# Kernel optimization log

Measured on AMD Instinct MI355X. Metric: run time of the kernel, lower is better.

Reference implementation:

```python
import jax, jax.numpy as jnp
import numpy as np

EMBED = 1024
HEADS = 16
HEAD_DIM = EMBED // HEADS
SCALE = HEAD_DIM ** (-0.5)
LN_EPS = 1e-5


def setup_inputs() -> dict:
    key = jax.random.key(0)
    ks = jax.random.split(key, 8)
    B, N = 2, 2048
    s = EMBED ** -0.5
    return {
        "x": jax.random.normal(ks[0], (B, N, EMBED), dtype=jnp.float32),
        "ln_w": jnp.ones((EMBED,), jnp.float32),
        "ln_b": jnp.zeros((EMBED,), jnp.float32),
        "Wq": jax.random.normal(ks[1], (EMBED, EMBED), jnp.float32) * s,
        "Wk": jax.random.normal(ks[2], (EMBED, EMBED), jnp.float32) * s,
        "Wv": jax.random.normal(ks[3], (EMBED, EMBED), jnp.float32) * s,
        "Wo": jax.random.normal(ks[4], (EMBED, EMBED), jnp.float32) * s,
        "bo": jnp.zeros((EMBED,), jnp.float32),
    }


def reference(x, ln_w, ln_b, Wq, Wk, Wv, Wo, bo):
    residual = x
    # LayerNorm (pre-norm)
    mu = jnp.mean(x, axis=-1, keepdims=True)
    var = jnp.mean(jnp.square(x - mu), axis=-1, keepdims=True)
    xn = (x - mu) * jax.lax.rsqrt(var + LN_EPS) * ln_w + ln_b

    B, N, _ = xn.shape
    q = (xn @ Wq.T).reshape(B, N, HEADS, HEAD_DIM).transpose(0, 2, 1, 3)  # b h n d
    k = (xn @ Wk.T).reshape(B, N, HEADS, HEAD_DIM).transpose(0, 2, 1, 3)
    v = (xn @ Wv.T).reshape(B, N, HEADS, HEAD_DIM).transpose(0, 2, 1, 3)

    dots = jnp.einsum('bhqd,bhkd->bhqk', q, k) * SCALE
    causal = jnp.tril(jnp.ones((N, N), dtype=bool))
    dots = jnp.where(causal, dots, -jnp.inf)
    attn = jax.nn.softmax(dots, axis=-1)
    out = jnp.einsum('bhqk,bhkd->bhqd', attn, v)
    out = out.transpose(0, 2, 1, 3).reshape(B, N, EMBED)
    # dropout is identity in eval mode
    return residual + out @ Wo.T + bo
```

## Files before the change

kernel.cpp:

```cpp
#include <hip/hip_runtime.h>

#define E 1024
#define NSEQ 2048
#define HEADS 16
#define HD 64

typedef unsigned short u16;
typedef short short8 __attribute__((ext_vector_type(8)));
typedef float f32x4 __attribute__((ext_vector_type(4)));

template<bool B> struct BC { static constexpr bool v = B; };

#define GLOAD_LDS16(gp, lp)                                        \
    __builtin_amdgcn_global_load_lds(                              \
        (const __attribute__((address_space(1))) void*)(gp),       \
        (__attribute__((address_space(3))) void*)(lp), 16, 0, 0)

__device__ __forceinline__ u16 f2bf(float f) {
    union { float f; unsigned u; } v; v.f = f;
    unsigned r = v.u + 0x7fffu + ((v.u >> 16) & 1u);
    return (u16)(r >> 16);
}

__device__ __forceinline__ unsigned cvt_pk_bf16(float lo, float hi) {
    unsigned r;
    asm("v_cvt_pk_bf16_f32 %0, %1, %2" : "=v"(r) : "v"(lo), "v"(hi));
    return r;
}

__device__ __forceinline__ f32x4 mfma16(short8 a, short8 b, f32x4 c) {
    return __builtin_amdgcn_mfma_f32_16x16x32_bf16(a, b, c, 0, 0, 0);
}

__global__ __launch_bounds__(256) void convw_k(
    const float* __restrict__ Wq, const float* __restrict__ Wk,
    const float* __restrict__ Wv, const float* __restrict__ Wo,
    u16* __restrict__ out)
{
    const unsigned i = (blockIdx.x * 256u + threadIdx.x) * 4u;
    const unsigned m = i >> 20;
    const float* src = (m == 0) ? Wq : (m == 1) ? Wk : (m == 2) ? Wv : Wo;
    const float4 v = *(const float4*)(src + (i & 0xFFFFFu));
    *(uint2*)(out + i) = make_uint2(
        ((unsigned)f2bf(v.x)) | (((unsigned)f2bf(v.y)) << 16),
        ((unsigned)f2bf(v.z)) | (((unsigned)f2bf(v.w)) << 16));
}

__global__ __launch_bounds__(256) void ln_fwd(
    const float* __restrict__ X, const float* __restrict__ w,
    const float* __restrict__ bb, u16* __restrict__ xn)
{
    const int row = blockIdx.x, tid = threadIdx.x;
    const int lane = tid & 63, wave = tid >> 6;
    const float4 v = ((const float4*)(X + (size_t)row * E))[tid];
    float s = v.x + v.y + v.z + v.w;
    float s2 = v.x * v.x + v.y * v.y + v.z * v.z + v.w * v.w;
#pragma unroll
    for (int off = 1; off < 64; off <<= 1) {
        s += __shfl_xor(s, off);
        s2 += __shfl_xor(s2, off);
    }
    __shared__ float red[8];
    if (lane == 0) { red[wave] = s; red[4 + wave] = s2; }
    __syncthreads();
    s = red[0] + red[1] + red[2] + red[3];
    s2 = red[4] + red[5] + red[6] + red[7];
    const float mu = s * (1.f / 1024.f);
    float var = s2 * (1.f / 1024.f) - mu * mu;
    var = fmaxf(var, 0.f);
    const float rs = rsqrtf(var + 1e-5f);
    const float4 wv = ((const float4*)w)[tid];
    const float4 bv = ((const float4*)bb)[tid];
    u16 o0 = f2bf((v.x - mu) * rs * wv.x + bv.x);
    u16 o1 = f2bf((v.y - mu) * rs * wv.y + bv.y);
    u16 o2 = f2bf((v.z - mu) * rs * wv.z + bv.z);
    u16 o3 = f2bf((v.w - mu) * rs * wv.w + bv.w);
    *(uint2*)(xn + (size_t)row * E + tid * 4) =
        make_uint2(((unsigned)o0) | (((unsigned)o1) << 16),
                   ((unsigned)o2) | (((unsigned)o3) << 16));
}

__global__ __launch_bounds__(256) void vtrans(
    const u16* __restrict__ Vb, u16* __restrict__ VT)
{
    __shared__ u16 tl[64][65];
    const int t = threadIdx.x;
    const int ntile = blockIdx.x, bh = blockIdx.y;
    const int b = bh >> 4, h = bh & 15;
    const int n0 = ntile * 64;
    {
        const int nl = t >> 2;
        const u16* src = Vb + ((size_t)b * NSEQ + n0 + nl) * E + h * 64;
#pragma unroll
        for (int u = 0; u < 2; ++u) {
            const int d0 = (t & 3) * 16 + u * 8;
            short8 v = *(const short8*)(src + d0);
#pragma unroll
            for (int j = 0; j < 8; ++j) tl[nl][d0 + j] = (u16)v[j];
        }
    }
    __syncthreads();
    {
        const int d = t >> 2, nc = (t & 3) * 16;
        u16* dst = VT + ((size_t)bh * 64 + d) * NSEQ + n0 + nc;
#pragma unroll
        for (int u = 0; u < 2; ++u) {
            short8 o;
#pragma unroll
            for (int j = 0; j < 8; ++j) o[j] = (short)tl[nc + u * 8 + j][d];
            *(short8*)(dst + u * 8) = o;
        }
    }
}

template<int MODE>
__global__ __launch_bounds__(256) void gemm_nt(
    const u16* __restrict__ A, const u16* __restrict__ Wbase,
    u16* __restrict__ outb, float* __restrict__ outf,
    const float* __restrict__ resid, const float* __restrict__ bias)
{
    __shared__ __align__(16) unsigned char As[128 * 128];
    __shared__ __align__(16) unsigned char Bs[128 * 128];
    const int tid = threadIdx.x;
    const int lane = tid & 63, wave = tid >> 6;
    const int l15 = lane & 15, l4 = lane >> 4;
    const int wm = wave >> 1, wn = wave & 1;
    const int nt = blockIdx.x, mt = blockIdx.y, z = blockIdx.z;
    const u16* Bw = Wbase + (size_t)z * (E * (size_t)E);

    const int lrow8 = lane >> 3;
    const int lchunk = (lane & 7) ^ lrow8;
    const u16* gA = A + (size_t)(mt * 128 + lrow8) * E + lchunk * 8;
    const u16* gB = Bw + (size_t)(nt * 128 + lrow8) * E + lchunk * 8;

    f32x4 acc[4][4] = {};

    for (int kt = 0; kt < 16; ++kt) {
#pragma unroll
        for (int i = 0; i < 4; ++i) {
            const int rb = (i * 4 + wave) * 8;
            GLOAD_LDS16(gA + (size_t)rb * E + kt * 64, As + rb * 128);
            GLOAD_LDS16(gB + (size_t)rb * E + kt * 64, Bs + rb * 128);
        }
        __syncthreads();
#pragma unroll
        for (int ks = 0; ks < 2; ++ks) {
            short8 af[4], bfr[4];
#pragma unroll
            for (int i = 0; i < 4; ++i) {
                int ra = wm * 64 + i * 16 + l15;
                af[i] = *(const short8*)(As + ra * 128 + ((ks * 64 + l4 * 16) ^ ((ra & 7) << 4)));
                int rb2 = wn * 64 + i * 16 + l15;
                bfr[i] = *(const short8*)(Bs + rb2 * 128 + ((ks * 64 + l4 * 16) ^ ((rb2 & 7) << 4)));
            }
#pragma unroll
            for (int i = 0; i < 4; ++i)
#pragma unroll
                for (int j = 0; j < 4; ++j)
                    acc[i][j] = mfma16(af[i], bfr[j], acc[i][j]);
        }
        __syncthreads();
    }

    const int orow0 = mt * 128 + wm * 64, ocol0 = nt * 128 + wn * 64;
    if (MODE == 0) {
        u16* outz = outb + (size_t)z * (4096 * (size_t)E);
        const float osc = (z == 0) ? 0.18033688f : 1.0f;
#pragma unroll
        for (int i = 0; i < 4; ++i)
#pragma unroll
            for (int j = 0; j < 4; ++j)
#pragma unroll
                for (int r = 0; r < 4; ++r) {
                    int row = orow0 + i * 16 + l4 * 4 + r;
                    int col = ocol0 + j * 16 + l15;
                    outz[(size_t)row * E + col] = f2bf(acc[i][j][r] * osc);
                }
    } else {
#pragma unroll
        for (int i = 0; i < 4; ++i)
#pragma unroll
            for (int j = 0; j < 4; ++j)
#pragma unroll
                for (int r = 0; r < 4; ++r) {
                    int row = orow0 + i * 16 + l4 * 4 + r;
                    int col = ocol0 + j * 16 + l15;
                    size_t idx = (size_t)row * E + col;
                    outf[idx] = acc[i][j][r] + resid[idx] + bias[col];
                }
    }
}

__global__ __launch_bounds__(256) void attn_fwd(
    const u16* __restrict__ Q, const u16* __restrict__ K,
    const u16* __restrict__ VT, u16* __restrict__ O)
{
    __shared__ __align__(16) unsigned char Kls[2 * 8192];
    __shared__ __align__(16) unsigned char Vls[2 * 8192];
    __shared__ __align__(16) unsigned char Ps[4 * 4096];
    const int tid = threadIdx.x, lane = tid & 63, wave = tid >> 6;
    const int l15 = lane & 15, l4 = lane >> 4;
    const int h = blockIdx.x, x = blockIdx.y, b = blockIdx.z;
    const int qe = b ? (15 - x) : x;
    const int qw0 = qe * 128 + wave * 32;
    const size_t bbase = (size_t)b * NSEQ * E + h * HD;
    const u16* vt = VT + ((size_t)(b * 16 + h) * 64) * NSEQ;
    const int ntiles = 2 * qe + 2;

    short8 aq[2][2];
#pragma unroll
    for (int qt = 0; qt < 2; ++qt)
#pragma unroll
        for (int ks = 0; ks < 2; ++ks)
            aq[qt][ks] = *(const short8*)(Q + bbase + (size_t)(qw0 + qt * 16 + l15) * E + ks * 32 + l4 * 8);

    f32x4 accO[2][4] = {};
    float mrow[2] = {-1e30f, -1e30f};
    float lrow[2] = {0.f, 0.f};

    unsigned char* Pw = Ps + wave * 4096;

    const int srow = lane >> 3;
    const int sc8 = ((lane & 7) ^ srow) * 8;
    auto stage = [&](int t, int buf) {
        const u16* Kg = K + bbase + (size_t)(t * 64) * E;
        const u16* vg = vt + t * 64;
        unsigned char* kd = Kls + buf * 8192 + wave * 1024;
        unsigned char* vd = Vls + buf * 8192 + wave * 1024;
#pragma unroll
        for (int i = 0; i < 2; ++i) {
            const int r = wave * 8 + srow + i * 32;
            GLOAD_LDS16(Kg + (size_t)r * E + sc8, kd + i * 4096);
            GLOAD_LDS16(vg + (size_t)r * NSEQ + sc8, vd + i * 4096);
        }
    };

    stage(0, 0);
    __syncthreads();

    auto step = [&](int t, auto mc) {
        constexpr bool MASK = decltype(mc)::v;
        const int buf = t & 1;
        if (t + 1 < ntiles) stage(t + 1, buf ^ 1);
        const unsigned char* Kc = Kls + buf * 8192;
        const unsigned char* Vc = Vls + buf * 8192;

        f32x4 s[2][4] = {};
#pragma unroll
        for (int kvt = 0; kvt < 4; ++kvt) {
            const int kr = kvt * 16 + l15;
#pragma unroll
            for (int ks = 0; ks < 2; ++ks) {
                short8 kfr = *(const short8*)(Kc + kr * 128 + ((ks * 64 + l4 * 16) ^ ((kr & 7) << 4)));
                s[0][kvt] = mfma16(kfr, aq[0][ks], s[0][kvt]);
                s[1][kvt] = mfma16(kfr, aq[1][ks], s[1][kvt]);
            }
        }

        if constexpr (MASK) {
#pragma unroll
            for (int qt = 0; qt < 2; ++qt) {
                const int qg = qw0 + qt * 16 + l15;
#pragma unroll
                for (int kvt = 0; kvt < 4; ++kvt)
#pragma unroll
                    for (int r = 0; r < 4; ++r) {
                        int kvg = t * 64 + kvt * 16 + l4 * 4 + r;
                        if (kvg > qg) s[qt][kvt][r] = -1e30f;
                    }
            }
        }

#pragma unroll
        for (int qt = 0; qt < 2; ++qt) {
            float m0 = fmaxf(fmaxf(s[qt][0][0], s[qt][0][1]), fmaxf(s[qt][0][2], s[qt][0][3]));
            float m1 = fmaxf(fmaxf(s[qt][1][0], s[qt][1][1]), fmaxf(s[qt][1][2], s[qt][1][3]));
            float m2 = fmaxf(fmaxf(s[qt][2][0], s[qt][2][1]), fmaxf(s[qt][2][2], s[qt][2][3]));
            float m3 = fmaxf(fmaxf(s[qt][3][0], s[qt][3][1]), fmaxf(s[qt][3][2], s[qt][3][3]));
            float pm = fmaxf(fmaxf(m0, m1), fmaxf(m2, m3));
            if (__any(pm > mrow[qt] + 8.f)) {
                pm = fmaxf(pm, __shfl_xor(pm, 16));
                pm = fmaxf(pm, __shfl_xor(pm, 32));
                const float mn = fmaxf(mrow[qt], pm);
                const float sc = exp2f(mrow[qt] - mn);
                mrow[qt] = mn;
                lrow[qt] *= sc;
#pragma unroll
                for (int r = 0; r < 4; ++r) {
                    float scv = __shfl(sc, l4 * 4 + r);
#pragma unroll
                    for (int dt = 0; dt < 4; ++dt) accO[qt][dt][r] *= scv;
                }
            }
            const int pr = qt * 16 + l15;
            const int sw = (l15 & 7) << 4;
#pragma unroll
            for (int kvt = 0; kvt < 4; ++kvt) {
                float p0 = exp2f(s[qt][kvt][0] - mrow[qt]);
                float p1 = exp2f(s[qt][kvt][1] - mrow[qt]);
                float p2 = exp2f(s[qt][kvt][2] - mrow[qt]);
                float p3 = exp2f(s[qt][kvt][3] - mrow[qt]);
                lrow[qt] += (p0 + p1) + (p2 + p3);
                uint2 pk = make_uint2(cvt_pk_bf16(p0, p1), cvt_pk_bf16(p2, p3));
                *(uint2*)(Pw + pr * 128 + ((kvt * 32 + l4 * 8) ^ sw)) = pk;
            }
        }

#pragma unroll
        for (int ks2 = 0; ks2 < 2; ++ks2) {
            const int cb = ks2 * 64 + l4 * 16;
            short8 pf0 = *(const short8*)(Pw + l15 * 128 + (cb ^ ((l15 & 7) << 4)));
            short8 pf1 = *(const short8*)(Pw + (16 + l15) * 128 + (cb ^ ((l15 & 7) << 4)));
#pragma unroll
            for (int dt = 0; dt < 4; ++dt) {
                const int vr = dt * 16 + l15;
                short8 vfr = *(const short8*)(Vc + vr * 128 + (cb ^ ((vr & 7) << 4)));
                accO[0][dt] = mfma16(pf0, vfr, accO[0][dt]);
                accO[1][dt] = mfma16(pf1, vfr, accO[1][dt]);
            }
        }
        __syncthreads();
    };

    int t = 0;
    for (; t < 2 * qe; ++t) step(t, BC<false>{});
    step(t, BC<true>{}); ++t;
    step(t, BC<true>{});

    float linv[2];
#pragma unroll
    for (int qt = 0; qt < 2; ++qt) {
        float tl2 = lrow[qt];
        tl2 += __shfl_xor(tl2, 16);
        tl2 += __shfl_xor(tl2, 32);
        linv[qt] = 1.f / tl2;
    }
#pragma unroll
    for (int rt = 0; rt < 2; ++rt)
#pragma unroll
        for (int r = 0; r < 4; ++r) {
            float lq = __shfl(linv[rt], l4 * 4 + r);
            const int qg = qw0 + rt * 16 + l4 * 4 + r;
#pragma unroll
            for (int dt = 0; dt < 4; ++dt)
                O[bbase + (size_t)qg * E + dt * 16 + l15] = f2bf(accO[rt][dt][r] * lq);
        }
}

extern "C" void kernel_launch(void* const* d_in, const int* in_sizes, int n_in,
                              void* d_out, int out_size, void* d_ws, size_t ws_size,
                              hipStream_t stream)
{
    const float* x    = (const float*)d_in[0];
    const float* ln_w = (const float*)d_in[1];
    const float* ln_b = (const float*)d_in[2];
    const float* Wq   = (const float*)d_in[3];
    const float* Wk   = (const float*)d_in[4];
    const float* Wv   = (const float*)d_in[5];
    const float* Wo   = (const float*)d_in[6];
    const float* bo   = (const float*)d_in[7];
    float* out = (float*)d_out;

    u16* ws  = (u16*)d_ws;
    u16* Wbf = ws;
    u16* xn  = Wbf + (size_t)4 * 1024 * 1024;
    u16* Qb  = xn + (size_t)4096 * 1024;
    u16* Kb  = Qb + (size_t)4096 * 1024;
    u16* Vb  = Kb + (size_t)4096 * 1024;
    u16* Ob  = Vb + (size_t)4096 * 1024;
    u16* VT  = xn;

    convw_k<<<dim3(4096), dim3(256), 0, stream>>>(Wq, Wk, Wv, Wo, Wbf);
    ln_fwd<<<dim3(4096), dim3(256), 0, stream>>>(x, ln_w, ln_b, xn);
    gemm_nt<0><<<dim3(8, 32, 3), dim3(256), 0, stream>>>(
        xn, Wbf, Qb, nullptr, nullptr, nullptr);
    vtrans<<<dim3(32, 32), dim3(256), 0, stream>>>(Vb, VT);
    attn_fwd<<<dim3(16, 16, 2), dim3(256), 0, stream>>>(Qb, Kb, VT, Ob);
    gemm_nt<1><<<dim3(8, 32, 1), dim3(256), 0, stream>>>(
        Ob, Wbf + (size_t)3 * 1024 * 1024, nullptr, out, x, bo);
}
```

Measured before the change: 132.6 us.

## Split KV range across wave pairs and pair causal strips per block

```diff
diff --git a/kernel.cpp b/kernel.cpp
--- a/kernel.cpp
+++ b/kernel.cpp
@@ -195,156 +195,197 @@
     const u16* __restrict__ Q, const u16* __restrict__ K,
     const u16* __restrict__ VT, u16* __restrict__ O)
 {
-    __shared__ __align__(16) unsigned char Kls[2 * 8192];
-    __shared__ __align__(16) unsigned char Vls[2 * 8192];
+    __shared__ __align__(16) unsigned char Kls[2 * 16384];
+    __shared__ __align__(16) unsigned char Vls[2 * 16384];
     __shared__ __align__(16) unsigned char Ps[4 * 4096];
     const int tid = threadIdx.x, lane = tid & 63, wave = tid >> 6;
+    const int sub = wave >> 1, par = wave & 1;
     const int l15 = lane & 15, l4 = lane >> 4;
-    const int h = blockIdx.x, x = blockIdx.y, b = blockIdx.z;
-    const int qe = b ? (15 - x) : x;
-    const int qw0 = qe * 128 + wave * 32;
+    const int h = blockIdx.x, j = blockIdx.y, b = blockIdx.z;
     const size_t bbase = (size_t)b * NSEQ * E + h * HD;
     const u16* vt = VT + ((size_t)(b * 16 + h) * 64) * NSEQ;
-    const int ntiles = 2 * qe + 2;
-
-    short8 aq[2][2];
-#pragma unroll
-    for (int qt = 0; qt < 2; ++qt)
-#pragma unroll
-        for (int ks = 0; ks < 2; ++ks)
-            aq[qt][ks] = *(const short8*)(Q + bbase + (size_t)(qw0 + qt * 16 + l15) * E + ks * 32 + l4 * 8);
-
-    f32x4 accO[2][4] = {};
-    float mrow[2] = {-1e30f, -1e30f};
-    float lrow[2] = {0.f, 0.f};
 
     unsigned char* Pw = Ps + wave * 4096;
-
-    const int srow = lane >> 3;
-    const int sc8 = ((lane & 7) ^ srow) * 8;
+    const int srowK = lane >> 3, kchunk = (lane & 7) ^ srowK;
+    const int srowV = lane >> 4, vchunk = (lane & 15) ^ (((wave & 1) << 2) + srowV);
+
     auto stage = [&](int t, int buf) {
-        const u16* Kg = K + bbase + (size_t)(t * 64) * E;
-        const u16* vg = vt + t * 64;
-        unsigned char* kd = Kls + buf * 8192 + wave * 1024;
-        unsigned char* vd = Vls + buf * 8192 + wave * 1024;
-#pragma unroll
-        for (int i = 0; i < 2; ++i) {
-            const int r = wave * 8 + srow + i * 32;
-            GLOAD_LDS16(Kg + (size_t)r * E + sc8, kd + i * 4096);
-            GLOAD_LDS16(vg + (size_t)r * NSEQ + sc8, vd + i * 4096);
-        }
+        const u16* Kg = K + bbase + (size_t)(t * 128) * E;
+        const u16* vg = vt + t * 128;
+        unsigned char* kd = Kls + buf * 16384 + wave * 1024;
+        unsigned char* vd = Vls + buf * 16384 + wave * 1024;
+#pragma unroll
+        for (int i = 0; i < 4; ++i)
+            GLOAD_LDS16(Kg + (size_t)(wave * 8 + i * 32 + srowK) * E + kchunk * 8, kd + i * 4096);
+#pragma unroll
+        for (int i = 0; i < 4; ++i)
+            GLOAD_LDS16(vg + (size_t)(wave * 4 + i * 16 + srowV) * NSEQ + vchunk * 8, vd + i * 4096);
     };
 
-    stage(0, 0);
-    __syncthreads();
-
-    auto step = [&](int t, auto mc) {
-        constexpr bool MASK = decltype(mc)::v;
-        const int buf = t & 1;
-        if (t + 1 < ntiles) stage(t + 1, buf ^ 1);
-        const unsigned char* Kc = Kls + buf * 8192;
-        const unsigned char* Vc = Vls + buf * 8192;
-
-        f32x4 s[2][4] = {};
-#pragma unroll
-        for (int kvt = 0; kvt < 4; ++kvt) {
-            const int kr = kvt * 16 + l15;
-#pragma unroll
-            for (int ks = 0; ks < 2; ++ks) {
-                short8 kfr = *(const short8*)(Kc + kr * 128 + ((ks * 64 + l4 * 16) ^ ((kr & 7) << 4)));
-                s[0][kvt] = mfma16(kfr, aq[0][ks], s[0][kvt]);
-                s[1][kvt] = mfma16(kfr, aq[1][ks], s[1][kvt]);
-            }
-        }
-
-        if constexpr (MASK) {
+    auto run_strip = [&](int jj) {
+        const int qw0 = jj * 64 + sub * 32;
+        const int R = (jj >> 1) + 1;
+
+        short8 aq[2][2];
+#pragma unroll
+        for (int qt = 0; qt < 2; ++qt)
+#pragma unroll
+            for (int ks = 0; ks < 2; ++ks)
+                aq[qt][ks] = *(const short8*)(Q + bbase + (size_t)(qw0 + qt * 16 + l15) * E + ks * 32 + l4 * 8);
+
+        f32x4 accO[2][4] = {};
+        float mrow[2] = {-5e29f, -5e29f};
+        float lrow[2] = {0.f, 0.f};
+
+        stage(0, 0);
+        __syncthreads();
+
+        auto step = [&](int t, auto mc) {
+            constexpr bool MASK = decltype(mc)::v;
+            const int buf = t & 1;
+            if (t + 1 < R) stage(t + 1, buf ^ 1);
+            const unsigned char* Kc = Kls + buf * 16384;
+            const unsigned char* Vc = Vls + buf * 16384;
+
+            f32x4 s[2][4] = {};
+#pragma unroll
+            for (int kvt = 0; kvt < 4; ++kvt) {
+                const int kr = par * 64 + kvt * 16 + l15;
+#pragma unroll
+                for (int ks = 0; ks < 2; ++ks) {
+                    short8 kfr = *(const short8*)(Kc + kr * 128 + ((ks * 64 + l4 * 16) ^ ((kr & 7) << 4)));
+                    s[0][kvt] = mfma16(kfr, aq[0][ks], s[0][kvt]);
+                    s[1][kvt] = mfma16(kfr, aq[1][ks], s[1][kvt]);
+                }
+            }
+
+            if constexpr (MASK) {
+#pragma unroll
+                for (int qt = 0; qt < 2; ++qt) {
+                    const int qg = qw0 + qt * 16 + l15;
+#pragma unroll
+                    for (int kvt = 0; kvt < 4; ++kvt)
+#pragma unroll
+                        for (int r = 0; r < 4; ++r) {
+                            int kvg = t * 128 + par * 64 + kvt * 16 + l4 * 4 + r;
+                            if (kvg > qg) s[qt][kvt][r] = -1e30f;
+                        }
+                }
+            }
+
 #pragma unroll
             for (int qt = 0; qt < 2; ++qt) {
-                const int qg = qw0 + qt * 16 + l15;
-#pragma unroll
-                for (int kvt = 0; kvt < 4; ++kvt)
+                float m0 = fmaxf(fmaxf(s[qt][0][0], s[qt][0][1]), fmaxf(s[qt][0][2], s[qt][0][3]));
+                float m1 = fmaxf(fmaxf(s[qt][1][0], s[qt][1][1]), fmaxf(s[qt][1][2], s[qt][1][3]));
+                float m2 = fmaxf(fmaxf(s[qt][2][0], s[qt][2][1]), fmaxf(s[qt][2][2], s[qt][2][3]));
+                float m3 = fmaxf(fmaxf(s[qt][3][0], s[qt][3][1]), fmaxf(s[qt][3][2], s[qt][3][3]));
+                float pm = fmaxf(fmaxf(m0, m1), fmaxf(m2, m3));
+                if (__any(pm > mrow[qt] + 8.f)) {
+                    pm = fmaxf(pm, __shfl_xor(pm, 16));
+                    pm = fmaxf(pm, __shfl_xor(pm, 32));
+                    const float mn = fmaxf(mrow[qt], pm);
+                    const float sc = exp2f(mrow[qt] - mn);
+                    mrow[qt] = mn;
+                    lrow[qt] *= sc;
 #pragma unroll
                     for (int r = 0; r < 4; ++r) {
-                        int kvg = t * 64 + kvt * 16 + l4 * 4 + r;
-                        if (kvg > qg) s[qt][kvt][r] = -1e30f;
+                        float scv = __shfl(sc, l4 * 4 + r);
+#pragma unroll
+                        for (int dt = 0; dt < 4; ++dt) accO[qt][dt][r] *= scv;
                     }
-            }
-        }
-
-#pragma unroll
-        for (int qt = 0; qt < 2; ++qt) {
-            float m0 = fmaxf(fmaxf(s[qt][0][0], s[qt][0][1]), fmaxf(s[qt][0][2], s[qt][0][3]));
-            float m1 = fmaxf(fmaxf(s[qt][1][0], s[qt][1][1]), fmaxf(s[qt][1][2], s[qt][1][3]));
-            float m2 = fmaxf(fmaxf(s[qt][2][0], s[qt][2][1]), fmaxf(s[qt][2][2], s[qt][2][3]));
-            float m3 = fmaxf(fmaxf(s[qt][3][0], s[qt][3][1]), fmaxf(s[qt][3][2], s[qt][3][3]));
-            float pm = fmaxf(fmaxf(m0, m1), fmaxf(m2, m3));
-            if (__any(pm > mrow[qt] + 8.f)) {
-                pm = fmaxf(pm, __shfl_xor(pm, 16));
-                pm = fmaxf(pm, __shfl_xor(pm, 32));
-                const float mn = fmaxf(mrow[qt], pm);
-                const float sc = exp2f(mrow[qt] - mn);
-                mrow[qt] = mn;
-                lrow[qt] *= sc;
+                }
+                const int pr = qt * 16 + l15;
+                const int sw = (l15 & 7) << 4;
+#pragma unroll
+                for (int kvt = 0; kvt < 4; ++kvt) {
+                    float p0 = exp2f(s[qt][kvt][0] - mrow[qt]);
+                    float p1 = exp2f(s[qt][kvt][1] - mrow[qt]);
+                    float p2 = exp2f(s[qt][kvt][2] - mrow[qt]);
+                    float p3 = exp2f(s[qt][kvt][3] - mrow[qt]);
+                    lrow[qt] += (p0 + p1) + (p2 + p3);
+                    uint2 pk = make_uint2(cvt_pk_bf16(p0, p1), cvt_pk_bf16(p2, p3));
+                    *(uint2*)(Pw + pr * 128 + ((kvt * 32 + l4 * 8) ^ sw)) = pk;
+                }
+            }
+
+#pragma unroll
+            for (int ks2 = 0; ks2 < 2; ++ks2) {
+                const int cb = ks2 * 64 + l4 * 16;
+                short8 pf0 = *(const short8*)(Pw + l15 * 128 + (cb ^ ((l15 & 7) << 4)));
+                short8 pf1 = *(const short8*)(Pw + (16 + l15) * 128 + (cb ^ ((l15 & 7) << 4)));
+#pragma unroll
+                for (int dt = 0; dt < 4; ++dt) {
+                    const int vr = dt * 16 + l15;
+                    short8 vfr = *(const short8*)(Vc + vr * 256 + ((par * 128 + cb) ^ ((vr & 7) << 4)));
+                    accO[0][dt] = mfma16(pf0, vfr, accO[0][dt]);
+                    accO[1][dt] = mfma16(pf1, vfr, accO[1][dt]);
+                }
+            }
+            __syncthreads();
+        };
+
+        for (int t = 0; t + 1 < R; ++t) step(t, BC<false>{});
+        step(R - 1, BC<true>{});
+
+        f32x4* Mg = (f32x4*)Kls;
+        if (par == 1) {
+            f32x4 hd;
+            hd[0] = mrow[0]; hd[1] = mrow[1]; hd[2] = lrow[0]; hd[3] = lrow[1];
+            Mg[(sub * 9) * 64 + lane] = hd;
+#pragma unroll
+            for (int qt = 0; qt < 2; ++qt)
+#pragma unroll
+                for (int dt = 0; dt < 4; ++dt)
+                    Mg[(sub * 9 + 1 + qt * 4 + dt) * 64 + lane] = accO[qt][dt];
+        }
+        __syncthreads();
+        if (par == 0) {
+            f32x4 hd = Mg[(sub * 9) * 64 + lane];
+            float scA[2], scB[2];
+#pragma unroll
+            for (int qt = 0; qt < 2; ++qt) {
+                const float mB = hd[qt], lB = hd[2 + qt];
+                const float ms = fmaxf(mrow[qt], mB);
+                scA[qt] = exp2f(mrow[qt] - ms);
+                scB[qt] = exp2f(mB - ms);
+                lrow[qt] = lrow[qt] * scA[qt] + lB * scB[qt];
+            }
+#pragma unroll
+            for (int qt = 0; qt < 2; ++qt)
 #pragma unroll
                 for (int r = 0; r < 4; ++r) {
-                    float scv = __shfl(sc, l4 * 4 + r);
-#pragma unroll
-                    for (int dt = 0; dt < 4; ++dt) accO[qt][dt][r] *= scv;
-                }
-            }
-            const int pr = qt * 16 + l15;
-            const int sw = (l15 & 7) << 4;
-#pragma unroll
-            for (int kvt = 0; kvt < 4; ++kvt) {
-                float p0 = exp2f(s[qt][kvt][0] - mrow[qt]);
-                float p1 = exp2f(s[qt][kvt][1] - mrow[qt]);
-                float p2 = exp2f(s[qt][kvt][2] - mrow[qt]);
-                float p3 = exp2f(s[qt][kvt][3] - mrow[qt]);
-                lrow[qt] += (p0 + p1) + (p2 + p3);
-                uint2 pk = make_uint2(cvt_pk_bf16(p0, p1), cvt_pk_bf16(p2, p3));
-                *(uint2*)(Pw + pr * 128 + ((kvt * 32 + l4 * 8) ^ sw)) = pk;
-            }
-        }
-
-#pragma unroll
-        for (int ks2 = 0; ks2 < 2; ++ks2) {
-            const int cb = ks2 * 64 + l4 * 16;
-            short8 pf0 = *(const short8*)(Pw + l15 * 128 + (cb ^ ((l15 & 7) << 4)));
-            short8 pf1 = *(const short8*)(Pw + (16 + l15) * 128 + (cb ^ ((l15 & 7) << 4)));
-#pragma unroll
-            for (int dt = 0; dt < 4; ++dt) {
-                const int vr = dt * 16 + l15;
-                short8 vfr = *(const short8*)(Vc + vr * 128 + (cb ^ ((vr & 7) << 4)));
-                accO[0][dt] = mfma16(pf0, vfr, accO[0][dt]);
-                accO[1][dt] = mfma16(pf1, vfr, accO[1][dt]);
-            }
+                    float sa = __shfl(scA[qt], l4 * 4 + r);
+                    float sb = __shfl(scB[qt], l4 * 4 + r);
+#pragma unroll
+                    for (int dt = 0; dt < 4; ++dt) {
+                        f32x4 ob = Mg[(sub * 9 + 1 + qt * 4 + dt) * 64 + lane];
+                        accO[qt][dt][r] = accO[qt][dt][r] * sa + ob[r] * sb;
+                    }
+                }
+            float linv[2];
+#pragma unroll
+            for (int qt = 0; qt < 2; ++qt) {
+                float tl2 = lrow[qt];
+                tl2 += __shfl_xor(tl2, 16);
+                tl2 += __shfl_xor(tl2, 32);
+                linv[qt] = 1.f / tl2;
+            }
+#pragma unroll
+            for (int rt = 0; rt < 2; ++rt)
+#pragma unroll
+                for (int r = 0; r < 4; ++r) {
+                    float lq = __shfl(linv[rt], l4 * 4 + r);
+                    const int qg = qw0 + rt * 16 + l4 * 4 + r;
+#pragma unroll
+                    for (int dt = 0; dt < 4; ++dt)
+                        O[bbase + (size_t)qg * E + dt * 16 + l15] = f2bf(accO[rt][dt][r] * lq);
+                }
         }
         __syncthreads();
     };
 
-    int t = 0;
-    for (; t < 2 * qe; ++t) step(t, BC<false>{});
-    step(t, BC<true>{}); ++t;
-    step(t, BC<true>{});
-
-    float linv[2];
-#pragma unroll
-    for (int qt = 0; qt < 2; ++qt) {
-        float tl2 = lrow[qt];
-        tl2 += __shfl_xor(tl2, 16);
-        tl2 += __shfl_xor(tl2, 32);
-        linv[qt] = 1.f / tl2;
-    }
-#pragma unroll
-    for (int rt = 0; rt < 2; ++rt)
-#pragma unroll
-        for (int r = 0; r < 4; ++r) {
-            float lq = __shfl(linv[rt], l4 * 4 + r);
-            const int qg = qw0 + rt * 16 + l4 * 4 + r;
-#pragma unroll
-            for (int dt = 0; dt < 4; ++dt)
-                O[bbase + (size_t)qg * E + dt * 16 + l15] = f2bf(accO[rt][dt][r] * lq);
-        }
+    run_strip(j);
+    run_strip(31 - j);
 }
 
 extern "C" void kernel_launch(void* const* d_in, const int* in_sizes, int n_in,
```

Result: faster. 122.4 us (-7.7%).
